# Optimization experiments

Hardware: AMD Instinct MI355X
Metric: run time of the kernel (lower is better)

## Reference

```python
import jax, jax.numpy as jnp
import numpy as np

B, T, IN, H, O = 128, 512, 512, 512, 128

def setup_inputs() -> dict:
    key = jax.random.key(0)
    ks = jax.random.split(key, 16)
    s = 1.0 / np.sqrt(H)
    u = lambda k, shape: jax.random.uniform(k, shape, jnp.float32, -s, s)
    return {
        "x": jax.random.normal(ks[0], (B, T, IN), jnp.float32),
        # PyTorch GRU layer 0: weight_ih_l0 [3H, IN] (gate order r,z,n)
        "W_ih0": u(ks[1], (3 * H, IN)), "W_hh0": u(ks[2], (3 * H, H)),
        "b_ih0": u(ks[3], (3 * H,)),   "b_hh0": u(ks[4], (3 * H,)),
        # layer 1
        "W_ih1": u(ks[5], (3 * H, H)), "W_hh1": u(ks[6], (3 * H, H)),
        "b_ih1": u(ks[7], (3 * H,)),   "b_hh1": u(ks[8], (3 * H,)),
        # fc: Linear(H, O); fc_cate: Linear(O, 3O)
        "W_fc": u(ks[9], (O, H)),      "b_fc": u(ks[10], (O,)),
        "W_fcc": jax.random.uniform(ks[11], (3 * O, O), jnp.float32, -1/np.sqrt(O), 1/np.sqrt(O)),
        "b_fcc": jax.random.uniform(ks[12], (3 * O,), jnp.float32, -1/np.sqrt(O), 1/np.sqrt(O)),
    }

def _gru_layer(x, W_ih, W_hh, b_ih, b_hh):
    # x: [B, T, D] -> hidden sequence [B, T, H]. PyTorch gate order: r, z, n.
    Bm, Tm, _ = x.shape
    Hm = W_hh.shape[1]
    # precompute input projections for all timesteps: [B, T, 3H]
    xg = jnp.einsum('btd,gd->btg', x, W_ih) + b_ih
    b_hr, b_hz, b_hn = jnp.split(b_hh, 3)
    def step(h, xg_t):
        hg = h @ W_hh.T                       # [B, 3H]
        xr, xz, xn = jnp.split(xg_t, 3, axis=-1)
        hr, hz, hn = jnp.split(hg, 3, axis=-1)
        r = jax.nn.sigmoid(xr + hr + b_hr)
        z = jax.nn.sigmoid(xz + hz + b_hz)
        n = jnp.tanh(xn + r * (hn + b_hn))
        h_new = (1.0 - z) * n + z * h
        return h_new, h_new
    h0 = jnp.zeros((Bm, Hm), x.dtype)
    _, hs = jax.lax.scan(step, h0, jnp.swapaxes(xg, 0, 1))  # [T, B, H]
    return jnp.swapaxes(hs, 0, 1)

def reference(x, W_ih0, W_hh0, b_ih0, b_hh0, W_ih1, W_hh1, b_ih1, b_hh1, W_fc, b_fc, W_fcc, b_fcc):
    h1 = _gru_layer(x, W_ih0, W_hh0, b_ih0, b_hh0)   # layer 0 (dropout=0.0)
    h2 = _gru_layer(h1, W_ih1, W_hh1, b_ih1, b_hh1)  # layer 1
    out = h2[:, -1] @ W_fc.T + b_fc                  # [B, O]
    out_cate = out @ W_fcc.T + b_fcc                 # [B, 3O]
    return out[:, None, :], out_cate.reshape(-1, O, 3)
```

## Files before the change

### kernel.cpp

```cpp
#include <hip/hip_runtime.h>

#define Tn 512
#define Hn 512
#define HS 65536
#define NBLK 256

typedef __attribute__((ext_vector_type(8))) short s8v;
typedef __attribute__((ext_vector_type(4))) float f4v;
typedef __attribute__((ext_vector_type(4))) unsigned u4v;
typedef unsigned long long ull;

__device__ __forceinline__ unsigned short f2bf(float f) {
  unsigned u = __float_as_uint(f);
  u = u + 0x7fffu + ((u >> 16) & 1u);
  return (unsigned short)(u >> 16);
}
__device__ __forceinline__ float bf2f(unsigned short s) {
  return __uint_as_float(((unsigned)s) << 16);
}
__device__ __forceinline__ float sigm(float v) { return 1.f / (1.f + __expf(-v)); }
__device__ __forceinline__ float tanh_f(float v) {
  v = fminf(fmaxf(v, -15.f), 15.f);
  float e = __expf(2.f * v);
  return (e - 1.f) / (e + 1.f);
}
__device__ __forceinline__ f4v mfma3(s8v ah, s8v al, s8v whh, s8v wll, f4v c) {
  c = __builtin_amdgcn_mfma_f32_16x16x32_bf16(ah, whh, c, 0, 0, 0);
  c = __builtin_amdgcn_mfma_f32_16x16x32_bf16(al, whh, c, 0, 0, 0);
  c = __builtin_amdgcn_mfma_f32_16x16x32_bf16(ah, wll, c, 0, 0, 0);
  return c;
}

__device__ __forceinline__ ull ld_mall64(const ull* p) {
  return __hip_atomic_load(p, __ATOMIC_RELAXED, __HIP_MEMORY_SCOPE_AGENT);
}
__device__ __forceinline__ void st_mall(unsigned* p, unsigned v) {
  __hip_atomic_store(p, v, __ATOMIC_RELAXED, __HIP_MEMORY_SCOPE_AGENT);
}

__device__ __forceinline__ void poll2(const int* pa, int ta, const int* pb2, int tb,
                                      int lane) {
  const int* p = (lane < 32) ? (pa + lane) : (pb2 + (lane - 32));
  const int tgt = (lane < 32) ? ta : tb;
  for (;;) {
    int v = (int)__hip_atomic_load(p, __ATOMIC_RELAXED, __HIP_MEMORY_SCOPE_AGENT);
    if (__all(v >= tgt)) break;
    __builtin_amdgcn_s_sleep(1);
  }
  asm volatile("" ::: "memory");
}

__global__ void __launch_bounds__(512) __attribute__((amdgpu_waves_per_eu(2, 2)))
gru_fused(
    const float* __restrict__ x,
    const float* __restrict__ Wih0, const float* __restrict__ Whh0,
    const float* __restrict__ bih0, const float* __restrict__ bhh0,
    const float* __restrict__ Wih1, const float* __restrict__ Whh1,
    const float* __restrict__ bih1, const float* __restrict__ bhh1,
    int* __restrict__ flags,
    unsigned* __restrict__ h1ring,
    unsigned* __restrict__ h2ring,
    float* __restrict__ h2fin) {
  __shared__ __align__(16) float smem[38912];
  float (*part)[64][28] = (float (*)[64][28])smem;

  const int tid = threadIdx.x, lane = tid & 63, wv = tid >> 6;
  const bool inside = (wv < 4);
  const int kq = wv & 3;
  const bool comb0 = (wv == 4), comb1 = (wv == 5);
  const int colr = lane & 15, kg = lane >> 4;

  const int bid = blockIdx.x;
  const int g = bid & 7;
  const int layer = g & 1;
  const int mq = g >> 1;
  const int jg = bid >> 3;
  const int col = jg * 16 + colr;

  s8v* const wlf = (s8v*)((char*)smem + 57344 + wv * 12288);

  const float* W = inside ? (layer ? Wih1 : Wih0) : (layer ? Whh1 : Whh0);
  s8v wh[3][4];
#pragma unroll
  for (int gg = 0; gg < 3; ++gg) {
    const float* wrow = W + (size_t)(gg * Hn + col) * Hn + kq * 128 + kg * 8;
#pragma unroll
    for (int ks = 0; ks < 4; ++ks) {
      s8v lov;
#pragma unroll
      for (int e = 0; e < 8; ++e) {
        float v = wrow[ks * 32 + e];
        unsigned short hi = f2bf(v);
        wh[gg][ks][e] = (short)hi;
        lov[e] = (short)f2bf(v - bf2f(hi));
      }
      wlf[(gg * 4 + ks) * 64 + lane] = lov;
    }
  }

  float brz = 0, bzz = 0, bin = 0, bhn = 0;
  if (comb0 || comb1) {
    const float* bi = layer ? bih1 : bih0;
    const float* bb = layer ? bhh1 : bhh0;
    brz = bi[col] + bb[col];
    bzz = bi[Hn + col] + bb[Hn + col];
    bin = bi[2 * Hn + col];
    bhn = bb[2 * Hn + col];
  }

  const bool is_xw = (layer == 0 && inside);

  float4 xp[2][4][2];
  if (is_xw) {
#pragma unroll
    for (int mt = 0; mt < 2; ++mt) {
      const int rowA = mq * 32 + mt * 16 + colr;
      const float* xq = x + ((size_t)rowA * Tn) * 512 + kq * 128 + kg * 8;
#pragma unroll
      for (int ks = 0; ks < 4; ++ks) {
        xp[mt][ks][0] = *(const float4*)(xq + ks * 32);
        xp[mt][ks][1] = *(const float4*)(xq + ks * 32 + 4);
      }
    }
  }

  int* const ownline = flags + g * 32;
  int* const l0line = flags + (mq * 2) * 32;
  int* const l1line = flags + (mq * 2 + 1) * 32;

  float hown[4] = {0.f, 0.f, 0.f, 0.f};

  __syncthreads();

#pragma unroll 1
  for (int t = 0; t < Tn; ++t) {
    if (layer == 0) {
      if (comb0 || comb1) poll2(ownline, 2 * t, l1line, 2 * (t - 3), lane);
      else if (!inside)   poll2(ownline, 2 * t, ownline, 2 * t, lane);
    } else {
      if (inside) poll2(l0line, 2 * (t + 1), l0line, 2 * (t + 1), lane);
      else        poll2(ownline, 2 * t, ownline, 2 * t, lane);
    }
    __syncthreads();

    f4v acc[2][3];
#pragma unroll
    for (int mt = 0; mt < 2; ++mt)
#pragma unroll
      for (int gg = 0; gg < 3; ++gg) acc[mt][gg] = (f4v){0.f, 0.f, 0.f, 0.f};

    if (is_xw) {
#pragma unroll
      for (int ks = 0; ks < 4; ++ks) {
        s8v wl0 = wlf[(0 * 4 + ks) * 64 + lane];
        s8v wl1 = wlf[(1 * 4 + ks) * 64 + lane];
        s8v wl2 = wlf[(2 * 4 + ks) * 64 + lane];
#pragma unroll
        for (int mt = 0; mt < 2; ++mt) {
          float v[8];
          v[0] = xp[mt][ks][0].x; v[1] = xp[mt][ks][0].y;
          v[2] = xp[mt][ks][0].z; v[3] = xp[mt][ks][0].w;
          v[4] = xp[mt][ks][1].x; v[5] = xp[mt][ks][1].y;
          v[6] = xp[mt][ks][1].z; v[7] = xp[mt][ks][1].w;
          u4v au, lu;
#pragma unroll
          for (int q = 0; q < 4; ++q) {
            unsigned u0 = __float_as_uint(v[2 * q]);
            unsigned u1 = __float_as_uint(v[2 * q + 1]);
            unsigned m0 = u0 & 0xffff0000u, m1 = u1 & 0xffff0000u;
            au[q] = (u0 >> 16) | m1;
            float l0 = v[2 * q] - __uint_as_float(m0);
            float l1 = v[2 * q + 1] - __uint_as_float(m1);
            lu[q] = (__float_as_uint(l0) >> 16) | (__float_as_uint(l1) & 0xffff0000u);
          }
          s8v ah = __builtin_bit_cast(s8v, au);
          s8v al = __builtin_bit_cast(s8v, lu);
          acc[mt][0] = mfma3(ah, al, wh[0][ks], wl0, acc[mt][0]);
          acc[mt][1] = mfma3(ah, al, wh[1][ks], wl1, acc[mt][1]);
          acc[mt][2] = mfma3(ah, al, wh[2][ks], wl2, acc[mt][2]);
        }
      }
#pragma unroll
      for (int mt = 0; mt < 2; ++mt)
#pragma unroll
        for (int gg = 0; gg < 3; ++gg)
          *(f4v*)&part[wv][lane][mt * 12 + gg * 4] = acc[mt][gg];
      const int tpre = (t + 1 < Tn) ? (t + 1) : (Tn - 1);
#pragma unroll
      for (int mt = 0; mt < 2; ++mt) {
        const int rowA = mq * 32 + mt * 16 + colr;
        const float* xq = x + ((size_t)rowA * Tn + tpre) * 512 + kq * 128 + kg * 8;
#pragma unroll
        for (int ks = 0; ks < 4; ++ks) {
          xp[mt][ks][0] = *(const float4*)(xq + ks * 32);
          xp[mt][ks][1] = *(const float4*)(xq + ks * 32 + 4);
        }
      }
    } else {
      const unsigned* src;
      if (inside)      src = h1ring + (size_t)(t & 3) * HS;
      else if (layer)  src = h2ring + (size_t)((t - 1) & 1) * HS;
      else             src = h1ring + (size_t)((t - 1) & 3) * HS;

      ull ub[2][16];
#pragma unroll
      for (int mt = 0; mt < 2; ++mt) {
        const int rowA = mq * 32 + mt * 16 + colr;
        const ull* pb64 = (const ull*)(src + (size_t)rowA * 512 + kq * 128 + kg * 8);
#pragma unroll
        for (int i = 0; i < 16; ++i)
          ub[mt][i] = ld_mall64(pb64 + (i >> 2) * 16 + (i & 3));
      }
#pragma unroll
      for (int ks = 0; ks < 4; ++ks) {
        s8v wl0 = wlf[(0 * 4 + ks) * 64 + lane];
        s8v wl1 = wlf[(1 * 4 + ks) * 64 + lane];
        s8v wl2 = wlf[(2 * 4 + ks) * 64 + lane];
#pragma unroll
        for (int mt = 0; mt < 2; ++mt) {
          u4v ahw, alw;
#pragma unroll
          for (int j = 0; j < 4; ++j) {
            unsigned a = (unsigned)ub[mt][ks * 4 + j];
            unsigned b = (unsigned)(ub[mt][ks * 4 + j] >> 32);
            ahw[j] = (a >> 16) | (b & 0xffff0000u);
            alw[j] = (a & 0xffffu) | (b << 16);
          }
          s8v AH = __builtin_bit_cast(s8v, ahw);
          s8v AL = __builtin_bit_cast(s8v, alw);
          acc[mt][0] = mfma3(AH, AL, wh[0][ks], wl0, acc[mt][0]);
          acc[mt][1] = mfma3(AH, AL, wh[1][ks], wl1, acc[mt][1]);
          acc[mt][2] = mfma3(AH, AL, wh[2][ks], wl2, acc[mt][2]);
        }
      }
      if (comb0) {
#pragma unroll
        for (int gg = 0; gg < 3; ++gg)
          *(f4v*)&part[4][lane][gg * 4] = acc[1][gg];
      } else if (comb1) {
#pragma unroll
        for (int gg = 0; gg < 3; ++gg)
          *(f4v*)&part[5][lane][gg * 4] = acc[0][gg];
      } else {
#pragma unroll
        for (int mt = 0; mt < 2; ++mt)
#pragma unroll
          for (int gg = 0; gg < 3; ++gg)
            *(f4v*)&part[wv][lane][mt * 12 + gg * 4] = acc[mt][gg];
      }
    }
    __syncthreads();

    if (comb0 || comb1) {
      const int mt = comb0 ? 0 : 1;
      const int moff = mt * 12;
      f4v xs[3], hsum[3];
#pragma unroll
      for (int gg = 0; gg < 3; ++gg) {
        xs[gg] = *(const f4v*)&part[0][lane][moff + gg * 4]
               + *(const f4v*)&part[1][lane][moff + gg * 4]
               + *(const f4v*)&part[2][lane][moff + gg * 4]
               + *(const f4v*)&part[3][lane][moff + gg * 4];
        hsum[gg] = acc[mt][gg]
                 + *(const f4v*)&part[comb0 ? 5 : 4][lane][gg * 4]
                 + *(const f4v*)&part[6][lane][moff + gg * 4]
                 + *(const f4v*)&part[7][lane][moff + gg * 4];
      }
      unsigned* od = layer ? (h2ring + (size_t)(t & 1) * HS)
                           : (h1ring + (size_t)(t & 3) * HS);
#pragma unroll
      for (int r = 0; r < 4; ++r) {
        float rr = sigm(xs[0][r] + hsum[0][r] + brz);
        float zz = sigm(xs[1][r] + hsum[1][r] + bzz);
        float nn = tanh_f(xs[2][r] + bin + rr * (hsum[2][r] + bhn));
        float h = (1.f - zz) * nn + zz * hown[r];
        hown[r] = h;
        const int row = mq * 32 + mt * 16 + kg * 4 + r;
        unsigned short hi = f2bf(h);
        unsigned pk = ((unsigned)hi << 16) | (unsigned)f2bf(h - bf2f(hi));
        st_mall(od + (size_t)row * 512 + col, pk);
        if (layer == 1 && t == Tn - 1) h2fin[(size_t)row * 512 + col] = h;
      }
      asm volatile("s_waitcnt vmcnt(0)" ::: "memory");
      if (lane == 0)
        __hip_atomic_fetch_add(ownline + jg, 1, __ATOMIC_RELAXED,
                               __HIP_MEMORY_SCOPE_AGENT);
    }
  }
}

__global__ __launch_bounds__(256) void fc_kernel(const float* __restrict__ h2,
                                                 const float* __restrict__ Wfc,
                                                 const float* __restrict__ bfc,
                                                 float* __restrict__ out) {
  int gid = blockIdx.x * 256 + threadIdx.x;
  int b = gid >> 7, o = gid & 127;
  const float* hp = h2 + (size_t)b * Hn;
  const float* wp = Wfc + (size_t)o * Hn;
  float acc = bfc[o];
#pragma unroll 8
  for (int k = 0; k < Hn; k += 4) {
    float4 h = *(const float4*)(hp + k);
    float4 w = *(const float4*)(wp + k);
    acc = fmaf(h.x, w.x, acc); acc = fmaf(h.y, w.y, acc);
    acc = fmaf(h.z, w.z, acc); acc = fmaf(h.w, w.w, acc);
  }
  out[gid] = acc;
}

__global__ __launch_bounds__(256) void fcc_kernel(const float* __restrict__ outv,
                                                  const float* __restrict__ Wfcc,
                                                  const float* __restrict__ bfcc,
                                                  float* __restrict__ oc) {
  int gid = blockIdx.x * 256 + threadIdx.x;
  int b = gid / 384, g = gid - b * 384;
  const float* op = outv + (size_t)b * 128;
  const float* wp = Wfcc + (size_t)g * 128;
  float acc = bfcc[g];
#pragma unroll 8
  for (int k = 0; k < 128; k += 4) {
    float4 o4 = *(const float4*)(op + k);
    float4 w4 = *(const float4*)(wp + k);
    acc = fmaf(o4.x, w4.x, acc); acc = fmaf(o4.y, w4.y, acc);
    acc = fmaf(o4.z, w4.z, acc); acc = fmaf(o4.w, w4.w, acc);
  }
  oc[gid] = acc;
}

extern "C" void kernel_launch(void* const* d_in, const int* in_sizes, int n_in,
                              void* d_out, int out_size, void* d_ws, size_t ws_size,
                              hipStream_t stream) {
  (void)in_sizes; (void)n_in; (void)out_size; (void)ws_size;
  const float* x    = (const float*)d_in[0];
  const float* Wih0 = (const float*)d_in[1];
  const float* Whh0 = (const float*)d_in[2];
  const float* bih0 = (const float*)d_in[3];
  const float* bhh0 = (const float*)d_in[4];
  const float* Wih1 = (const float*)d_in[5];
  const float* Whh1 = (const float*)d_in[6];
  const float* bih1 = (const float*)d_in[7];
  const float* bhh1 = (const float*)d_in[8];
  const float* Wfc  = (const float*)d_in[9];
  const float* bfc  = (const float*)d_in[10];
  const float* Wfcc = (const float*)d_in[11];
  const float* bfcc = (const float*)d_in[12];

  char* w = (char*)d_ws;
  int* flags = (int*)w;
  unsigned* h1ring = (unsigned*)(w + 8192);
  unsigned* h2ring = h1ring + 4 * HS;
  float* h2fin = (float*)(h2ring + 2 * HS);
  const size_t total = 8192 + (size_t)4 * HS * 4 + (size_t)2 * HS * 4 + (size_t)HS * 4;

  hipMemsetAsync(d_ws, 0, total, stream);

  gru_fused<<<NBLK, 512, 0, stream>>>(x, Wih0, Whh0, bih0, bhh0,
                                      Wih1, Whh1, bih1, bhh1,
                                      flags, h1ring, h2ring, h2fin);

  float* out = (float*)d_out;
  fc_kernel<<<64, 256, 0, stream>>>(h2fin, Wfc, bfc, out);
  fcc_kernel<<<192, 256, 0, stream>>>(out, Wfcc, bfcc, out + 16384);
}
```

Before: 5.168 ms.

## Use a single combine wave and single-wave polling with monotonic step flags

Two combiner waves, each finishing one 16-row tile, become one wave that combines both tiles. The per-block flag counter, bumped twice per step by atomic add, becomes a plain store of the step index. Polling moves from several waves per block to wave 0 alone, with the block barrier releasing the rest, and layer 1's input waits now go through the peer flag line. This cuts atomic traffic and redundant polling, but the combine and gate math now runs serially in one wave, which may lengthen the critical path of each step.

```diff
diff --git a/kernel.cpp b/kernel.cpp
--- a/kernel.cpp
+++ b/kernel.cpp
@@ -36,18 +36,6 @@
 }
 __device__ __forceinline__ void st_mall(unsigned* p, unsigned v) {
   __hip_atomic_store(p, v, __ATOMIC_RELAXED, __HIP_MEMORY_SCOPE_AGENT);
-}
-
-__device__ __forceinline__ void poll2(const int* pa, int ta, const int* pb2, int tb,
-                                      int lane) {
-  const int* p = (lane < 32) ? (pa + lane) : (pb2 + (lane - 32));
-  const int tgt = (lane < 32) ? ta : tb;
-  for (;;) {
-    int v = (int)__hip_atomic_load(p, __ATOMIC_RELAXED, __HIP_MEMORY_SCOPE_AGENT);
-    if (__all(v >= tgt)) break;
-    __builtin_amdgcn_s_sleep(1);
-  }
-  asm volatile("" ::: "memory");
 }
 
 __global__ void __launch_bounds__(512) __attribute__((amdgpu_waves_per_eu(2, 2)))
@@ -67,7 +55,7 @@
   const int tid = threadIdx.x, lane = tid & 63, wv = tid >> 6;
   const bool inside = (wv < 4);
   const int kq = wv & 3;
-  const bool comb0 = (wv == 4), comb1 = (wv == 5);
+  const bool comb = (wv == 4);
   const int colr = lane & 15, kg = lane >> 4;
 
   const int bid = blockIdx.x;
@@ -99,7 +87,7 @@
   }
 
   float brz = 0, bzz = 0, bin = 0, bhn = 0;
-  if (comb0 || comb1) {
+  if (comb) {
     const float* bi = layer ? bih1 : bih0;
     const float* bb = layer ? bhh1 : bhh0;
     brz = bi[col] + bb[col];
@@ -125,21 +113,25 @@
   }
 
   int* const ownline = flags + g * 32;
-  int* const l0line = flags + (mq * 2) * 32;
-  int* const l1line = flags + (mq * 2 + 1) * 32;
-
-  float hown[4] = {0.f, 0.f, 0.f, 0.f};
+  int* const peerline = flags + (g ^ 1) * 32;
+
+  float hown[2][4] = {{0.f, 0.f, 0.f, 0.f}, {0.f, 0.f, 0.f, 0.f}};
 
   __syncthreads();
 
 #pragma unroll 1
   for (int t = 0; t < Tn; ++t) {
-    if (layer == 0) {
-      if (comb0 || comb1) poll2(ownline, 2 * t, l1line, 2 * (t - 3), lane);
-      else if (!inside)   poll2(ownline, 2 * t, ownline, 2 * t, lane);
-    } else {
-      if (inside) poll2(l0line, 2 * (t + 1), l0line, 2 * (t + 1), lane);
-      else        poll2(ownline, 2 * t, ownline, 2 * t, lane);
+    if (wv == 0) {
+      const int ta = t;
+      const int tb = layer ? (t + 1) : (t - 3);
+      const int* p = (lane < 32) ? (ownline + lane) : (peerline + (lane - 32));
+      const int tgt = (lane < 32) ? ta : tb;
+      for (;;) {
+        int v = __hip_atomic_load(p, __ATOMIC_RELAXED, __HIP_MEMORY_SCOPE_AGENT);
+        if (__all(v >= tgt)) break;
+        __builtin_amdgcn_s_sleep(1);
+      }
+      asm volatile("" ::: "memory");
     }
     __syncthreads();
 
@@ -233,15 +225,7 @@
           acc[mt][2] = mfma3(AH, AL, wh[2][ks], wl2, acc[mt][2]);
         }
       }
-      if (comb0) {
-#pragma unroll
-        for (int gg = 0; gg < 3; ++gg)
-          *(f4v*)&part[4][lane][gg * 4] = acc[1][gg];
-      } else if (comb1) {
-#pragma unroll
-        for (int gg = 0; gg < 3; ++gg)
-          *(f4v*)&part[5][lane][gg * 4] = acc[0][gg];
-      } else {
+      if (!comb) {
 #pragma unroll
         for (int mt = 0; mt < 2; ++mt)
 #pragma unroll
@@ -251,40 +235,41 @@
     }
     __syncthreads();
 
-    if (comb0 || comb1) {
-      const int mt = comb0 ? 0 : 1;
-      const int moff = mt * 12;
-      f4v xs[3], hsum[3];
-#pragma unroll
-      for (int gg = 0; gg < 3; ++gg) {
-        xs[gg] = *(const f4v*)&part[0][lane][moff + gg * 4]
-               + *(const f4v*)&part[1][lane][moff + gg * 4]
-               + *(const f4v*)&part[2][lane][moff + gg * 4]
-               + *(const f4v*)&part[3][lane][moff + gg * 4];
-        hsum[gg] = acc[mt][gg]
-                 + *(const f4v*)&part[comb0 ? 5 : 4][lane][gg * 4]
-                 + *(const f4v*)&part[6][lane][moff + gg * 4]
-                 + *(const f4v*)&part[7][lane][moff + gg * 4];
-      }
+    if (comb) {
       unsigned* od = layer ? (h2ring + (size_t)(t & 1) * HS)
                            : (h1ring + (size_t)(t & 3) * HS);
 #pragma unroll
-      for (int r = 0; r < 4; ++r) {
-        float rr = sigm(xs[0][r] + hsum[0][r] + brz);
-        float zz = sigm(xs[1][r] + hsum[1][r] + bzz);
-        float nn = tanh_f(xs[2][r] + bin + rr * (hsum[2][r] + bhn));
-        float h = (1.f - zz) * nn + zz * hown[r];
-        hown[r] = h;
-        const int row = mq * 32 + mt * 16 + kg * 4 + r;
-        unsigned short hi = f2bf(h);
-        unsigned pk = ((unsigned)hi << 16) | (unsigned)f2bf(h - bf2f(hi));
-        st_mall(od + (size_t)row * 512 + col, pk);
-        if (layer == 1 && t == Tn - 1) h2fin[(size_t)row * 512 + col] = h;
+      for (int mt = 0; mt < 2; ++mt) {
+        const int moff = mt * 12;
+        f4v xs[3], hsum[3];
+#pragma unroll
+        for (int gg = 0; gg < 3; ++gg) {
+          xs[gg] = *(const f4v*)&part[0][lane][moff + gg * 4]
+                 + *(const f4v*)&part[1][lane][moff + gg * 4]
+                 + *(const f4v*)&part[2][lane][moff + gg * 4]
+                 + *(const f4v*)&part[3][lane][moff + gg * 4];
+          hsum[gg] = acc[mt][gg]
+                   + *(const f4v*)&part[5][lane][moff + gg * 4]
+                   + *(const f4v*)&part[6][lane][moff + gg * 4]
+                   + *(const f4v*)&part[7][lane][moff + gg * 4];
+        }
+#pragma unroll
+        for (int r = 0; r < 4; ++r) {
+          float rr = sigm(xs[0][r] + hsum[0][r] + brz);
+          float zz = sigm(xs[1][r] + hsum[1][r] + bzz);
+          float nn = tanh_f(xs[2][r] + bin + rr * (hsum[2][r] + bhn));
+          float h = (1.f - zz) * nn + zz * hown[mt][r];
+          hown[mt][r] = h;
+          const int row = mq * 32 + mt * 16 + kg * 4 + r;
+          unsigned short hi = f2bf(h);
+          unsigned pk = ((unsigned)hi << 16) | (unsigned)f2bf(h - bf2f(hi));
+          st_mall(od + (size_t)row * 512 + col, pk);
+          if (layer == 1 && t == Tn - 1) h2fin[(size_t)row * 512 + col] = h;
+        }
       }
       asm volatile("s_waitcnt vmcnt(0)" ::: "memory");
       if (lane == 0)
-        __hip_atomic_fetch_add(ownline + jg, 1, __ATOMIC_RELAXED,
-                               __HIP_MEMORY_SCOPE_AGENT);
+        st_mall((unsigned*)(ownline + jg), (unsigned)(t + 1));
     }
   }
 }
```

Result: slower. 5.872 ms (+13.6%).
